# Kernel optimization log

Measured on AMD Instinct MI355X. Metric: run time of the kernel, lower is better.

The kernel has to match this reference:

```python
import jax, jax.numpy as jnp
import numpy as np

DEPTH = 8
LEAVES = 2 ** DEPTH            # 256 leaf values
N_NODES = 2 ** DEPTH - 1       # 255 internal split nodes
TEMP = 1.0
EPS_P = 1e-5
EPS_V = 1e-10
EPS_MASK = 1e-12


def setup_inputs() -> dict:
    key = jax.random.key(0)
    k1, k2, k3 = jax.random.split(key, 3)
    B, D, O = 8192, 512, 64
    x = jax.random.normal(k1, (B, D), dtype=jnp.float32)
    # BaseSplitter assumed: single linear layer + temperature sigmoid
    Ws = jax.random.normal(k2, (D, N_NODES), dtype=jnp.float32) * (1.0 / np.sqrt(D))
    bs = jnp.zeros((N_NODES,), dtype=jnp.float32)
    # xavier_uniform_ init for leaf value table (LEAVES, O)
    limit = float(np.sqrt(6.0 / (LEAVES + O)))
    value = jax.random.uniform(k3, (LEAVES, O), dtype=jnp.float32, minval=-limit, maxval=limit)
    return {"x": x, "Ws": Ws, "bs": bs, "value": value}


def _sdt_forward(x, Ws, bs, value):
    B = x.shape[0]
    leaves = value.shape[0]
    # splitter: per-node routing probabilities, shape (B, 2^depth - 1)
    probs = jax.nn.sigmoid((x @ Ws + bs) / TEMP)

    accum = jnp.zeros((B, leaves), dtype=jnp.float32)
    reg = jnp.float32(0.0)
    for d in range(DEPTH):  # small fixed loop over tree depth
        s, e = 2 ** d - 1, 2 ** (d + 1) - 1
        p = probs[:, s:e]                     # (B, 2^d) nodes at depth d
        logp = jnp.log(jnp.clip(p, EPS_P))
        log1mp = jnp.log(jnp.clip(1.0 - p, EPS_P))
        # regularization: sum over nodes of mean over batch
        reg = reg + (-0.5) * (2.0 ** (-d)) * jnp.log(jnp.clip(p * (1.0 - p), EPS_P)).mean(axis=0).sum()
        # interleave [logp_i, log1mp_i] per node, then broadcast each entry
        # over its span of leaves/2^(d+1) leaf slots
        contrib = jnp.stack([logp, log1mp], axis=-1).reshape(B, 2 ** (d + 1))
        rep = leaves // (2 ** (d + 1))
        accum = accum + jnp.broadcast_to(contrib[:, :, None], (B, 2 ** (d + 1), rep)).reshape(B, leaves)

    sign = jnp.sign(value)                                    # (L, O)
    logval = jnp.log(jnp.clip(jnp.abs(value), EPS_V))          # (L, O)
    ret = logval[None, :, :] + accum[:, :, None]               # (B, L, O)
    log_pos = jax.nn.logsumexp(ret + jnp.log((sign > 0).astype(jnp.float32) + EPS_MASK), axis=1)
    log_neg = jax.nn.logsumexp(ret + jnp.log((sign < 0).astype(jnp.float32) + EPS_MASK), axis=1)
    out = jnp.exp(log_pos) - jnp.exp(log_neg)                  # (B, O)
    return out, reg


def reference(x, Ws, bs, value):
    return _sdt_forward(x, Ws, bs, value)
```

## Files before the change

kernel.cpp:

```cpp
#include <hip/hip_runtime.h>


typedef __attribute__((ext_vector_type(8))) short short8;
typedef __attribute__((ext_vector_type(4))) float floatx4;

constexpr int D = 512, NN = 255, O = 64, M_BLK = 32;
constexpr int XPAD = 40;

__device__ __forceinline__ short f2bf(float f) {
  unsigned u = __builtin_bit_cast(unsigned, f);
  u += 0x7fffu + ((u >> 16) & 1u);
  return (short)(u >> 16);
}
__device__ __forceinline__ float bf2f(short h) {
  unsigned u = ((unsigned)(unsigned short)h) << 16;
  return __builtin_bit_cast(float, u);
}
__device__ __forceinline__ int pk2(short a, short b) {
  return (int)((unsigned short)a | ((unsigned)(unsigned short)b << 16));
}

__global__ void sdt_pre(const float* __restrict__ Ws, short* __restrict__ wth,
                        short* __restrict__ wtl, float* __restrict__ reg_slot) {
  int k = blockIdx.x;
  int n = threadIdx.x;
  float f = (n < NN) ? Ws[k * NN + n] : 0.f;
  short h = f2bf(f);
  short l = f2bf(f - bf2f(h));
  wth[n * D + k] = h;
  wtl[n * D + k] = l;
  if (k == 0 && n == 0) *reg_slot = 0.f;
}

__global__ __launch_bounds__(512, 2) void sdt_main(
    const float* __restrict__ x, const short* __restrict__ wth,
    const short* __restrict__ wtl, const float* __restrict__ bs,
    const float* __restrict__ value, float* __restrict__ out,
    float* __restrict__ reg_out)
{
  __shared__ short xh_s[M_BLK * XPAD];
  __shared__ short xl_s[M_BLK * XPAD];
  __shared__ float L_s[M_BLK * 260];
  __shared__ float P_s[M_BLK * 260];
  __shared__ float red_s[8];

  const int t = threadIdx.x;
  const int lane = t & 63, w = t >> 6;
  const int q = lane >> 4, r16 = lane & 15;
  const int R0 = blockIdx.x * M_BLK;

  const int nb0 = (w * 32 + r16) * D + q * 8;
  const int nb1 = (w * 32 + 16 + r16) * D + q * 8;
  const int aoff0 = (r16) * XPAD + q * 8;
  const int aoff1 = (16 + r16) * XPAD + q * 8;
  const int xr = t >> 3, xq = t & 7;
  const float* xg = x + (size_t)(R0 + xr) * D + xq * 4;

  floatx4 acc00 = {0,0,0,0}, acc01 = {0,0,0,0}, acc10 = {0,0,0,0}, acc11 = {0,0,0,0};
  short8 bh[3][2], bl[3][2];
  float4 xf[3];
  int xph0 = 0, xph1 = 0, xpl0 = 0, xpl1 = 0;

#pragma unroll
  for (int s = 0; s < 2; ++s) {
    bh[s][0] = *(const short8*)(wth + nb0 + s * 32);
    bl[s][0] = *(const short8*)(wtl + nb0 + s * 32);
    bh[s][1] = *(const short8*)(wth + nb1 + s * 32);
    bl[s][1] = *(const short8*)(wtl + nb1 + s * 32);
  }
  if (t < 256) {
    xf[0] = *(const float4*)(xg + 0 * 32);
    xf[1] = *(const float4*)(xg + 1 * 32);
    xf[2] = *(const float4*)(xg + 2 * 32);
    short h0 = f2bf(xf[0].x), h1 = f2bf(xf[0].y), h2 = f2bf(xf[0].z), h3 = f2bf(xf[0].w);
    short l0 = f2bf(xf[0].x - bf2f(h0)), l1 = f2bf(xf[0].y - bf2f(h1));
    short l2 = f2bf(xf[0].z - bf2f(h2)), l3 = f2bf(xf[0].w - bf2f(h3));
    *(int*)&xh_s[xr * XPAD + xq * 4]     = pk2(h0, h1);
    *(int*)&xh_s[xr * XPAD + xq * 4 + 2] = pk2(h2, h3);
    *(int*)&xl_s[xr * XPAD + xq * 4]     = pk2(l0, l1);
    *(int*)&xl_s[xr * XPAD + xq * 4 + 2] = pk2(l2, l3);
  }
  __syncthreads();

#pragma unroll
  for (int c = 0; c < 16; ++c) {
    const int s0 = c % 3, s1 = (c + 1) % 3, s2 = (c + 2) % 3, s3 = (c + 3) % 3;
    if (c + 2 < 16) {
      bh[s2][0] = *(const short8*)(wth + nb0 + (c + 2) * 32);
      bl[s2][0] = *(const short8*)(wtl + nb0 + (c + 2) * 32);
      bh[s2][1] = *(const short8*)(wth + nb1 + (c + 2) * 32);
      bl[s2][1] = *(const short8*)(wtl + nb1 + (c + 2) * 32);
    }
    if (c + 3 < 16 && t < 256) xf[s3] = *(const float4*)(xg + (c + 3) * 32);

    short8 ah0 = *(const short8*)&xh_s[aoff0];
    short8 al0 = *(const short8*)&xl_s[aoff0];
    short8 ah1 = *(const short8*)&xh_s[aoff1];
    short8 al1 = *(const short8*)&xl_s[aoff1];

    acc00 = __builtin_amdgcn_mfma_f32_16x16x32_bf16(ah0, bh[s0][0], acc00, 0, 0, 0);
    acc01 = __builtin_amdgcn_mfma_f32_16x16x32_bf16(ah0, bh[s0][1], acc01, 0, 0, 0);
    acc10 = __builtin_amdgcn_mfma_f32_16x16x32_bf16(ah1, bh[s0][0], acc10, 0, 0, 0);
    acc11 = __builtin_amdgcn_mfma_f32_16x16x32_bf16(ah1, bh[s0][1], acc11, 0, 0, 0);
    acc00 = __builtin_amdgcn_mfma_f32_16x16x32_bf16(ah0, bl[s0][0], acc00, 0, 0, 0);
    acc01 = __builtin_amdgcn_mfma_f32_16x16x32_bf16(ah0, bl[s0][1], acc01, 0, 0, 0);
    acc10 = __builtin_amdgcn_mfma_f32_16x16x32_bf16(ah1, bl[s0][0], acc10, 0, 0, 0);
    acc11 = __builtin_amdgcn_mfma_f32_16x16x32_bf16(ah1, bl[s0][1], acc11, 0, 0, 0);
    acc00 = __builtin_amdgcn_mfma_f32_16x16x32_bf16(al0, bh[s0][0], acc00, 0, 0, 0);
    acc01 = __builtin_amdgcn_mfma_f32_16x16x32_bf16(al0, bh[s0][1], acc01, 0, 0, 0);
    acc10 = __builtin_amdgcn_mfma_f32_16x16x32_bf16(al1, bh[s0][0], acc10, 0, 0, 0);
    acc11 = __builtin_amdgcn_mfma_f32_16x16x32_bf16(al1, bh[s0][1], acc11, 0, 0, 0);

    if (c + 1 < 16 && t < 256) {
      float4 xv = xf[s1];
      short h0 = f2bf(xv.x), h1 = f2bf(xv.y), h2 = f2bf(xv.z), h3 = f2bf(xv.w);
      short l0 = f2bf(xv.x - bf2f(h0)), l1 = f2bf(xv.y - bf2f(h1));
      short l2 = f2bf(xv.z - bf2f(h2)), l3 = f2bf(xv.w - bf2f(h3));
      xph0 = pk2(h0, h1); xph1 = pk2(h2, h3);
      xpl0 = pk2(l0, l1); xpl1 = pk2(l2, l3);
    }
    __syncthreads();
    if (c + 1 < 16 && t < 256) {
      *(int*)&xh_s[xr * XPAD + xq * 4]     = xph0;
      *(int*)&xh_s[xr * XPAD + xq * 4 + 2] = xph1;
      *(int*)&xl_s[xr * XPAD + xq * 4]     = xpl0;
      *(int*)&xl_s[xr * XPAD + xq * 4 + 2] = xpl1;
    }
    __syncthreads();
  }

  {
#pragma unroll
    for (int r = 0; r < 4; ++r) {
      int row0 = q * 4 + r, row1 = 16 + q * 4 + r;
      int c0 = w * 32 + r16, c1 = w * 32 + 16 + r16;
      L_s[row0 * 260 + c0] = acc00[r];
      L_s[row0 * 260 + c1] = acc01[r];
      L_s[row1 * 260 + c0] = acc10[r];
      L_s[row1 * 260 + c1] = acc11[r];
    }
  }
  __syncthreads();

  const int col = t & 255, half = t >> 8;
  float rsum = 0.f;
  if (col < NN) {
    float b = bs[col];
    for (int r = half * 16; r < half * 16 + 16; ++r) {
      float z = L_s[r * 260 + col] + b;
      float p = 1.f / (1.f + __expf(-z));
      L_s[r * 260 + col] = p;
      rsum += __logf(fmaxf(p * (1.f - p), 1e-5f));
    }
    int dd = 31 - __clz(col + 1);
    rsum *= -0.5f / (8192.0f * (float)(1 << dd));
  }
#pragma unroll
  for (int off = 32; off; off >>= 1) rsum += __shfl_down(rsum, off, 64);
  if (lane == 0) red_s[w] = rsum;
  __syncthreads();
  if (t == 0) {
    float s = 0.f;
#pragma unroll
    for (int i = 0; i < 8; ++i) s += red_s[i];
    atomicAdd(reg_out, s);
  }

  {
    const int leaf = col;
    for (int r = half * 16; r < half * 16 + 16; ++r) {
      const float* Lr = &L_s[r * 260];
      float P = 1.f;
#pragma unroll
      for (int dd = 0; dd < 8; ++dd) {
        int node = (1 << dd) - 1 + (leaf >> (8 - dd));
        float p = Lr[node];
        float br = ((leaf >> (7 - dd)) & 1) ? (1.f - p) : p;
        P *= fmaxf(br, 1e-5f);
      }
      P_s[r * 260 + leaf] = P;
    }
  }
  __syncthreads();

  {
    const int o = t & 63, g = t >> 6;
    float a0 = 0.f, a1 = 0.f, a2 = 0.f, a3 = 0.f;
    const float* Pb = &P_s[(g * 4) * 260];
    for (int l4 = 0; l4 < 64; ++l4) {
      float v0 = value[(l4 * 4 + 0) * O + o];
      float v1 = value[(l4 * 4 + 1) * O + o];
      float v2 = value[(l4 * 4 + 2) * O + o];
      float v3 = value[(l4 * 4 + 3) * O + o];
      float4 p0 = *(const float4*)&Pb[0 * 260 + l4 * 4];
      float4 p1 = *(const float4*)&Pb[1 * 260 + l4 * 4];
      float4 p2 = *(const float4*)&Pb[2 * 260 + l4 * 4];
      float4 p3 = *(const float4*)&Pb[3 * 260 + l4 * 4];
      a0 += p0.x * v0 + p0.y * v1 + p0.z * v2 + p0.w * v3;
      a1 += p1.x * v0 + p1.y * v1 + p1.z * v2 + p1.w * v3;
      a2 += p2.x * v0 + p2.y * v1 + p2.z * v2 + p2.w * v3;
      a3 += p3.x * v0 + p3.y * v1 + p3.z * v2 + p3.w * v3;
    }
    out[(size_t)(R0 + g * 4 + 0) * O + o] = a0;
    out[(size_t)(R0 + g * 4 + 1) * O + o] = a1;
    out[(size_t)(R0 + g * 4 + 2) * O + o] = a2;
    out[(size_t)(R0 + g * 4 + 3) * O + o] = a3;
  }
}

extern "C" void kernel_launch(void* const* d_in, const int* in_sizes, int n_in,
                              void* d_out, int out_size, void* d_ws, size_t ws_size,
                              hipStream_t stream) {
  const float* x     = (const float*)d_in[0];
  const float* Ws    = (const float*)d_in[1];
  const float* bs    = (const float*)d_in[2];
  const float* value = (const float*)d_in[3];
  float* outp = (float*)d_out;
  float* reg_slot = outp + (size_t)8192 * O;
  short* wth = (short*)d_ws;
  short* wtl = wth + 256 * 512;

  sdt_pre<<<512, 256, 0, stream>>>(Ws, wth, wtl, reg_slot);
  sdt_main<<<8192 / M_BLK, 512, 0, stream>>>(x, wth, wtl, bs, value, outp, reg_slot);
}
```

Before: 100.1 us.

## Load x directly into registers, factor leaf products, and use bf16 MFMA for value matmul

The first GEMM now loads x straight from global memory into MFMA operand registers and converts it to hi/lo bf16 in-register. This removes the shared-memory staging and the two barriers per K step, but each wave now redundantly loads and converts the same x tile. Leaf path probabilities are computed per group of 8 leaves with a shared prefix product over the upper tree levels and stored as bf16. The final P×value contraction moves from scalar FMA over fp32 to bf16 MFMA using a value table transposed and converted in the pre-kernel, which lowers the precision of that second product.

```diff
diff --git a/kernel.cpp b/kernel.cpp
--- a/kernel.cpp
+++ b/kernel.cpp
@@ -4,8 +4,9 @@
 typedef __attribute__((ext_vector_type(8))) short short8;
 typedef __attribute__((ext_vector_type(4))) float floatx4;
 
-constexpr int D = 512, NN = 255, O = 64, M_BLK = 32;
-constexpr int XPAD = 40;
+constexpr int O = 64;
+constexpr int PSTR = 280;
+constexpr int LSTR = 260;
 
 __device__ __forceinline__ short f2bf(float f) {
   unsigned u = __builtin_bit_cast(unsigned, f);
@@ -16,148 +17,122 @@
   unsigned u = ((unsigned)(unsigned short)h) << 16;
   return __builtin_bit_cast(float, u);
 }
-__device__ __forceinline__ int pk2(short a, short b) {
-  return (int)((unsigned short)a | ((unsigned)(unsigned short)b << 16));
-}
-
-__global__ void sdt_pre(const float* __restrict__ Ws, short* __restrict__ wth,
-                        short* __restrict__ wtl, float* __restrict__ reg_slot) {
-  int k = blockIdx.x;
-  int n = threadIdx.x;
-  float f = (n < NN) ? Ws[k * NN + n] : 0.f;
+__device__ __forceinline__ void cvt8(float4 a, float4 b, short8& h, short8& l) {
+  float f[8] = {a.x, a.y, a.z, a.w, b.x, b.y, b.z, b.w};
+#pragma unroll
+  for (int i = 0; i < 8; ++i) {
+    short hh = f2bf(f[i]);
+    h[i] = hh;
+    l[i] = f2bf(f[i] - bf2f(hh));
+  }
+}
+
+__global__ void sdt_pre(const float* __restrict__ Ws, const float* __restrict__ value,
+                        short* __restrict__ wth, short* __restrict__ wtl,
+                        short* __restrict__ vt, float* __restrict__ reg_slot) {
+  int n = blockIdx.x;
+  int k = threadIdx.x;
+  float f = (n < 255) ? Ws[k * 255 + n] : 0.f;
   short h = f2bf(f);
-  short l = f2bf(f - bf2f(h));
-  wth[n * D + k] = h;
-  wtl[n * D + k] = l;
-  if (k == 0 && n == 0) *reg_slot = 0.f;
+  wth[n * 512 + k] = h;
+  wtl[n * 512 + k] = f2bf(f - bf2f(h));
+  if (n < 64 && k < 256) vt[n * 256 + k] = f2bf(value[k * O + n]);
+  if (n == 0 && k == 0) *reg_slot = 0.f;
 }
 
 __global__ __launch_bounds__(512, 2) void sdt_main(
     const float* __restrict__ x, const short* __restrict__ wth,
-    const short* __restrict__ wtl, const float* __restrict__ bs,
-    const float* __restrict__ value, float* __restrict__ out,
+    const short* __restrict__ wtl, const short* __restrict__ vt,
+    const float* __restrict__ bs, float* __restrict__ out,
     float* __restrict__ reg_out)
 {
-  __shared__ short xh_s[M_BLK * XPAD];
-  __shared__ short xl_s[M_BLK * XPAD];
-  __shared__ float L_s[M_BLK * 260];
-  __shared__ float P_s[M_BLK * 260];
+  __shared__ float L_s[32 * LSTR];
+  __shared__ short P_bf[32 * PSTR];
   __shared__ float red_s[8];
 
-  const int t = threadIdx.x;
-  const int lane = t & 63, w = t >> 6;
+  const int t = threadIdx.x, lane = t & 63, w = t >> 6;
   const int q = lane >> 4, r16 = lane & 15;
-  const int R0 = blockIdx.x * M_BLK;
-
-  const int nb0 = (w * 32 + r16) * D + q * 8;
-  const int nb1 = (w * 32 + 16 + r16) * D + q * 8;
-  const int aoff0 = (r16) * XPAD + q * 8;
-  const int aoff1 = (16 + r16) * XPAD + q * 8;
-  const int xr = t >> 3, xq = t & 7;
-  const float* xg = x + (size_t)(R0 + xr) * D + xq * 4;
+  const int R0 = blockIdx.x * 32;
+
+  const short* pwh0 = wth + (size_t)(w * 32 + r16) * 512 + q * 8;
+  const short* pwl0 = wtl + (size_t)(w * 32 + r16) * 512 + q * 8;
+  const short* pwh1 = pwh0 + 16 * 512;
+  const short* pwl1 = pwl0 + 16 * 512;
+  const float* px0 = x + (size_t)(R0 + r16) * 512 + q * 8;
+  const float* px1 = px0 + 16 * 512;
 
   floatx4 acc00 = {0,0,0,0}, acc01 = {0,0,0,0}, acc10 = {0,0,0,0}, acc11 = {0,0,0,0};
-  short8 bh[3][2], bl[3][2];
-  float4 xf[3];
-  int xph0 = 0, xph1 = 0, xpl0 = 0, xpl1 = 0;
-
-#pragma unroll
-  for (int s = 0; s < 2; ++s) {
-    bh[s][0] = *(const short8*)(wth + nb0 + s * 32);
-    bl[s][0] = *(const short8*)(wtl + nb0 + s * 32);
-    bh[s][1] = *(const short8*)(wth + nb1 + s * 32);
-    bl[s][1] = *(const short8*)(wtl + nb1 + s * 32);
-  }
-  if (t < 256) {
-    xf[0] = *(const float4*)(xg + 0 * 32);
-    xf[1] = *(const float4*)(xg + 1 * 32);
-    xf[2] = *(const float4*)(xg + 2 * 32);
-    short h0 = f2bf(xf[0].x), h1 = f2bf(xf[0].y), h2 = f2bf(xf[0].z), h3 = f2bf(xf[0].w);
-    short l0 = f2bf(xf[0].x - bf2f(h0)), l1 = f2bf(xf[0].y - bf2f(h1));
-    short l2 = f2bf(xf[0].z - bf2f(h2)), l3 = f2bf(xf[0].w - bf2f(h3));
-    *(int*)&xh_s[xr * XPAD + xq * 4]     = pk2(h0, h1);
-    *(int*)&xh_s[xr * XPAD + xq * 4 + 2] = pk2(h2, h3);
-    *(int*)&xl_s[xr * XPAD + xq * 4]     = pk2(l0, l1);
-    *(int*)&xl_s[xr * XPAD + xq * 4 + 2] = pk2(l2, l3);
+
+  short8 Bh0 = *(const short8*)(pwh0), Bl0 = *(const short8*)(pwl0);
+  short8 Bh1 = *(const short8*)(pwh1), Bl1 = *(const short8*)(pwl1);
+  float4 Xa0 = *(const float4*)(px0),  Xb0 = *(const float4*)(px0 + 4);
+  float4 Xa1 = *(const float4*)(px1),  Xb1 = *(const float4*)(px1 + 4);
+
+#pragma unroll
+  for (int c = 0; c < 16; ++c) {
+    short8 nh0, nl0, nh1, nl1;
+    float4 na0, nb0, na1, nb1;
+    if (c < 15) {
+      const int o = (c + 1) * 32;
+      nh0 = *(const short8*)(pwh0 + o); nl0 = *(const short8*)(pwl0 + o);
+      nh1 = *(const short8*)(pwh1 + o); nl1 = *(const short8*)(pwl1 + o);
+      na0 = *(const float4*)(px0 + o);  nb0 = *(const float4*)(px0 + o + 4);
+      na1 = *(const float4*)(px1 + o);  nb1 = *(const float4*)(px1 + o + 4);
+    }
+    short8 ah0, al0, ah1, al1;
+    cvt8(Xa0, Xb0, ah0, al0);
+    cvt8(Xa1, Xb1, ah1, al1);
+
+    acc00 = __builtin_amdgcn_mfma_f32_16x16x32_bf16(ah0, Bh0, acc00, 0, 0, 0);
+    acc01 = __builtin_amdgcn_mfma_f32_16x16x32_bf16(ah0, Bh1, acc01, 0, 0, 0);
+    acc10 = __builtin_amdgcn_mfma_f32_16x16x32_bf16(ah1, Bh0, acc10, 0, 0, 0);
+    acc11 = __builtin_amdgcn_mfma_f32_16x16x32_bf16(ah1, Bh1, acc11, 0, 0, 0);
+    acc00 = __builtin_amdgcn_mfma_f32_16x16x32_bf16(ah0, Bl0, acc00, 0, 0, 0);
+    acc01 = __builtin_amdgcn_mfma_f32_16x16x32_bf16(ah0, Bl1, acc01, 0, 0, 0);
+    acc10 = __builtin_amdgcn_mfma_f32_16x16x32_bf16(ah1, Bl0, acc10, 0, 0, 0);
+    acc11 = __builtin_amdgcn_mfma_f32_16x16x32_bf16(ah1, Bl1, acc11, 0, 0, 0);
+    acc00 = __builtin_amdgcn_mfma_f32_16x16x32_bf16(al0, Bh0, acc00, 0, 0, 0);
+    acc01 = __builtin_amdgcn_mfma_f32_16x16x32_bf16(al0, Bh1, acc01, 0, 0, 0);
+    acc10 = __builtin_amdgcn_mfma_f32_16x16x32_bf16(al1, Bh0, acc10, 0, 0, 0);
+    acc11 = __builtin_amdgcn_mfma_f32_16x16x32_bf16(al1, Bh1, acc11, 0, 0, 0);
+
+    if (c < 15) {
+      Bh0 = nh0; Bl0 = nl0; Bh1 = nh1; Bl1 = nl1;
+      Xa0 = na0; Xb0 = nb0; Xa1 = na1; Xb1 = nb1;
+    }
+  }
+
+  {
+    const int c0 = w * 32 + r16, c1 = c0 + 16;
+#pragma unroll
+    for (int r = 0; r < 4; ++r) {
+      int row0 = q * 4 + r, row1 = row0 + 16;
+      L_s[row0 * LSTR + c0] = acc00[r];
+      L_s[row0 * LSTR + c1] = acc01[r];
+      L_s[row1 * LSTR + c0] = acc10[r];
+      L_s[row1 * LSTR + c1] = acc11[r];
+    }
   }
   __syncthreads();
 
-#pragma unroll
-  for (int c = 0; c < 16; ++c) {
-    const int s0 = c % 3, s1 = (c + 1) % 3, s2 = (c + 2) % 3, s3 = (c + 3) % 3;
-    if (c + 2 < 16) {
-      bh[s2][0] = *(const short8*)(wth + nb0 + (c + 2) * 32);
-      bl[s2][0] = *(const short8*)(wtl + nb0 + (c + 2) * 32);
-      bh[s2][1] = *(const short8*)(wth + nb1 + (c + 2) * 32);
-      bl[s2][1] = *(const short8*)(wtl + nb1 + (c + 2) * 32);
-    }
-    if (c + 3 < 16 && t < 256) xf[s3] = *(const float4*)(xg + (c + 3) * 32);
-
-    short8 ah0 = *(const short8*)&xh_s[aoff0];
-    short8 al0 = *(const short8*)&xl_s[aoff0];
-    short8 ah1 = *(const short8*)&xh_s[aoff1];
-    short8 al1 = *(const short8*)&xl_s[aoff1];
-
-    acc00 = __builtin_amdgcn_mfma_f32_16x16x32_bf16(ah0, bh[s0][0], acc00, 0, 0, 0);
-    acc01 = __builtin_amdgcn_mfma_f32_16x16x32_bf16(ah0, bh[s0][1], acc01, 0, 0, 0);
-    acc10 = __builtin_amdgcn_mfma_f32_16x16x32_bf16(ah1, bh[s0][0], acc10, 0, 0, 0);
-    acc11 = __builtin_amdgcn_mfma_f32_16x16x32_bf16(ah1, bh[s0][1], acc11, 0, 0, 0);
-    acc00 = __builtin_amdgcn_mfma_f32_16x16x32_bf16(ah0, bl[s0][0], acc00, 0, 0, 0);
-    acc01 = __builtin_amdgcn_mfma_f32_16x16x32_bf16(ah0, bl[s0][1], acc01, 0, 0, 0);
-    acc10 = __builtin_amdgcn_mfma_f32_16x16x32_bf16(ah1, bl[s0][0], acc10, 0, 0, 0);
-    acc11 = __builtin_amdgcn_mfma_f32_16x16x32_bf16(ah1, bl[s0][1], acc11, 0, 0, 0);
-    acc00 = __builtin_amdgcn_mfma_f32_16x16x32_bf16(al0, bh[s0][0], acc00, 0, 0, 0);
-    acc01 = __builtin_amdgcn_mfma_f32_16x16x32_bf16(al0, bh[s0][1], acc01, 0, 0, 0);
-    acc10 = __builtin_amdgcn_mfma_f32_16x16x32_bf16(al1, bh[s0][0], acc10, 0, 0, 0);
-    acc11 = __builtin_amdgcn_mfma_f32_16x16x32_bf16(al1, bh[s0][1], acc11, 0, 0, 0);
-
-    if (c + 1 < 16 && t < 256) {
-      float4 xv = xf[s1];
-      short h0 = f2bf(xv.x), h1 = f2bf(xv.y), h2 = f2bf(xv.z), h3 = f2bf(xv.w);
-      short l0 = f2bf(xv.x - bf2f(h0)), l1 = f2bf(xv.y - bf2f(h1));
-      short l2 = f2bf(xv.z - bf2f(h2)), l3 = f2bf(xv.w - bf2f(h3));
-      xph0 = pk2(h0, h1); xph1 = pk2(h2, h3);
-      xpl0 = pk2(l0, l1); xpl1 = pk2(l2, l3);
-    }
-    __syncthreads();
-    if (c + 1 < 16 && t < 256) {
-      *(int*)&xh_s[xr * XPAD + xq * 4]     = xph0;
-      *(int*)&xh_s[xr * XPAD + xq * 4 + 2] = xph1;
-      *(int*)&xl_s[xr * XPAD + xq * 4]     = xpl0;
-      *(int*)&xl_s[xr * XPAD + xq * 4 + 2] = xpl1;
-    }
-    __syncthreads();
-  }
-
-  {
-#pragma unroll
-    for (int r = 0; r < 4; ++r) {
-      int row0 = q * 4 + r, row1 = 16 + q * 4 + r;
-      int c0 = w * 32 + r16, c1 = w * 32 + 16 + r16;
-      L_s[row0 * 260 + c0] = acc00[r];
-      L_s[row0 * 260 + c1] = acc01[r];
-      L_s[row1 * 260 + c0] = acc10[r];
-      L_s[row1 * 260 + c1] = acc11[r];
-    }
-  }
-  __syncthreads();
-
-  const int col = t & 255, half = t >> 8;
-  float rsum = 0.f;
-  if (col < NN) {
-    float b = bs[col];
-    for (int r = half * 16; r < half * 16 + 16; ++r) {
-      float z = L_s[r * 260 + col] + b;
-      float p = 1.f / (1.f + __expf(-z));
-      L_s[r * 260 + col] = p;
-      rsum += __logf(fmaxf(p * (1.f - p), 1e-5f));
-    }
-    int dd = 31 - __clz(col + 1);
-    rsum *= -0.5f / (8192.0f * (float)(1 << dd));
-  }
-#pragma unroll
-  for (int off = 32; off; off >>= 1) rsum += __shfl_down(rsum, off, 64);
-  if (lane == 0) red_s[w] = rsum;
+  {
+    const int col = t & 255, half = t >> 8;
+    float rsum = 0.f;
+    if (col < 255) {
+      float b = bs[col];
+      for (int r = half * 16; r < half * 16 + 16; ++r) {
+        float z = L_s[r * LSTR + col] + b;
+        float p = 1.f / (1.f + __expf(-z));
+        L_s[r * LSTR + col] = p;
+        rsum += __logf(fmaxf(p * (1.f - p), 1e-5f));
+      }
+      int dd = 31 - __clz(col + 1);
+      rsum *= -0.5f / (8192.0f * (float)(1 << dd));
+    }
+#pragma unroll
+    for (int off = 32; off; off >>= 1) rsum += __shfl_down(rsum, off, 64);
+    if (lane == 0) red_s[w] = rsum;
+  }
   __syncthreads();
   if (t == 0) {
     float s = 0.f;
@@ -167,44 +142,57 @@
   }
 
   {
-    const int leaf = col;
-    for (int r = half * 16; r < half * 16 + 16; ++r) {
-      const float* Lr = &L_s[r * 260];
-      float P = 1.f;
-#pragma unroll
-      for (int dd = 0; dd < 8; ++dd) {
-        int node = (1 << dd) - 1 + (leaf >> (8 - dd));
-        float p = Lr[node];
-        float br = ((leaf >> (7 - dd)) & 1) ? (1.f - p) : p;
-        P *= fmaxf(br, 1e-5f);
+    const int g8 = t & 31, rp = t >> 5;
+    const int Lb = g8 * 8;
+#pragma unroll
+    for (int rr = 0; rr < 2; ++rr) {
+      const int row = rp * 2 + rr;
+      const float* Lr = &L_s[row * LSTR];
+      float pre = 1.f;
+#pragma unroll
+      for (int dd = 0; dd < 5; ++dd) {
+        float p = Lr[(1 << dd) - 1 + (Lb >> (8 - dd))];
+        float br = ((Lb >> (7 - dd)) & 1) ? (1.f - p) : p;
+        pre *= fmaxf(br, 1e-5f);
       }
-      P_s[r * 260 + leaf] = P;
+      float p5 = Lr[31 + g8];
+      float s5a = fmaxf(p5, 1e-5f), s5b = fmaxf(1.f - p5, 1e-5f);
+      float p6a = Lr[63 + 2 * g8], p6b = Lr[63 + 2 * g8 + 1];
+      float p7v[4];
+#pragma unroll
+      for (int m = 0; m < 4; ++m) p7v[m] = Lr[127 + 4 * g8 + m];
+      short8 ph;
+#pragma unroll
+      for (int j = 0; j < 8; ++j) {
+        float s5 = (j & 4) ? s5b : s5a;
+        float p6 = (j & 4) ? p6b : p6a;
+        float s6 = fmaxf((j & 2) ? (1.f - p6) : p6, 1e-5f);
+        float p7 = p7v[j >> 1];
+        float s7 = fmaxf((j & 1) ? (1.f - p7) : p7, 1e-5f);
+        ph[j] = f2bf(pre * s5 * s6 * s7);
+      }
+      *(short8*)&P_bf[row * PSTR + Lb] = ph;
     }
   }
   __syncthreads();
 
   {
-    const int o = t & 63, g = t >> 6;
-    float a0 = 0.f, a1 = 0.f, a2 = 0.f, a3 = 0.f;
-    const float* Pb = &P_s[(g * 4) * 260];
-    for (int l4 = 0; l4 < 64; ++l4) {
-      float v0 = value[(l4 * 4 + 0) * O + o];
-      float v1 = value[(l4 * 4 + 1) * O + o];
-      float v2 = value[(l4 * 4 + 2) * O + o];
-      float v3 = value[(l4 * 4 + 3) * O + o];
-      float4 p0 = *(const float4*)&Pb[0 * 260 + l4 * 4];
-      float4 p1 = *(const float4*)&Pb[1 * 260 + l4 * 4];
-      float4 p2 = *(const float4*)&Pb[2 * 260 + l4 * 4];
-      float4 p3 = *(const float4*)&Pb[3 * 260 + l4 * 4];
-      a0 += p0.x * v0 + p0.y * v1 + p0.z * v2 + p0.w * v3;
-      a1 += p1.x * v0 + p1.y * v1 + p1.z * v2 + p1.w * v3;
-      a2 += p2.x * v0 + p2.y * v1 + p2.z * v2 + p2.w * v3;
-      a3 += p3.x * v0 + p3.y * v1 + p3.z * v2 + p3.w * v3;
-    }
-    out[(size_t)(R0 + g * 4 + 0) * O + o] = a0;
-    out[(size_t)(R0 + g * 4 + 1) * O + o] = a1;
-    out[(size_t)(R0 + g * 4 + 2) * O + o] = a2;
-    out[(size_t)(R0 + g * 4 + 3) * O + o] = a3;
+    const int tm = w & 1, tn = w >> 1;
+    floatx4 C = {0, 0, 0, 0};
+    const short* vb = vt + (size_t)(tn * 16 + r16) * 256 + q * 8;
+    const short* pa = &P_bf[(tm * 16 + r16) * PSTR + q * 8];
+#pragma unroll
+    for (int kc = 0; kc < 8; ++kc) {
+      short8 A8 = *(const short8*)(pa + kc * 32);
+      short8 B8 = *(const short8*)(vb + kc * 32);
+      C = __builtin_amdgcn_mfma_f32_16x16x32_bf16(A8, B8, C, 0, 0, 0);
+    }
+    const int col = tn * 16 + r16;
+#pragma unroll
+    for (int r = 0; r < 4; ++r) {
+      int row = tm * 16 + q * 4 + r;
+      out[(size_t)(R0 + row) * O + col] = C[r];
+    }
   }
 }
 
@@ -219,7 +207,8 @@
   float* reg_slot = outp + (size_t)8192 * O;
   short* wth = (short*)d_ws;
   short* wtl = wth + 256 * 512;
-
-  sdt_pre<<<512, 256, 0, stream>>>(Ws, wth, wtl, reg_slot);
-  sdt_main<<<8192 / M_BLK, 512, 0, stream>>>(x, wth, wtl, bs, value, outp, reg_slot);
-}
+  short* vt  = wtl + 256 * 512;
+
+  sdt_pre<<<256, 512, 0, stream>>>(Ws, value, wth, wtl, vt, reg_slot);
+  sdt_main<<<256, 512, 0, stream>>>(x, wth, wtl, vt, bs, outp, reg_slot);
+}
```

New measurement: 107.2 us. +7.1%, slower.
